# Performance work log

Measured on AMD Instinct MI355X. Metric: run time of the kernel, lower is better.

The kernel has to match this reference:

```python
import jax, jax.numpy as jnp
import numpy as np

B, T, O, H, CTX, HOR = 32, 24, 128, 512, 256, 48
MAX_STEP = 2.0


def setup_inputs() -> dict:
    key = jax.random.key(0)
    ks = jax.random.split(key, 20)
    def lin(k, out_d, in_d):
        bound = 1.0 / np.sqrt(in_d)
        kw, kb = jax.random.split(k)
        W = jax.random.uniform(kw, (out_d, in_d), jnp.float32, -bound, bound)
        b = jax.random.uniform(kb, (out_d,), jnp.float32, -bound, bound)
        return W, b
    W_emb, b_emb = lin(ks[0], H, 2)
    W_ctx, b_ctx = lin(ks[1], H, CTX)
    Wi_enc, bi_enc = lin(ks[2], 3 * H, H)
    Wh_enc, bh_enc = lin(ks[3], 3 * H, H)
    Wi_cell, bi_cell = lin(ks[4], 3 * H, H)
    Wh_cell, bh_cell = lin(ks[5], 3 * H, H)
    W1, b1 = lin(ks[6], H, H)
    W2, b2 = lin(ks[7], 2, H)
    z_ctx = jax.random.normal(ks[8], (B, CTX), jnp.float32)
    traj_hist = jax.random.uniform(ks[9], (B, T, O, 2), jnp.float32) * 10.0
    return dict(z_ctx=z_ctx, traj_hist=traj_hist,
                W_emb=W_emb, b_emb=b_emb, W_ctx=W_ctx, b_ctx=b_ctx,
                Wi_enc=Wi_enc, Wh_enc=Wh_enc, bi_enc=bi_enc, bh_enc=bh_enc,
                Wi_cell=Wi_cell, Wh_cell=Wh_cell, bi_cell=bi_cell, bh_cell=bh_cell,
                W1=W1, b1=b1, W2=W2, b2=b2, horizon=HOR)


def _gru(h, x, Wi, Wh, bi, bh):
    # PyTorch GRU gate math: gates ordered (r, z, n)
    gi = x @ Wi.T + bi  # [N, 3H]
    gh = h @ Wh.T + bh
    ir, iz, inn = jnp.split(gi, 3, axis=-1)
    hr, hz, hn = jnp.split(gh, 3, axis=-1)
    r = jax.nn.sigmoid(ir + hr)
    z = jax.nn.sigmoid(iz + hz)
    n = jnp.tanh(inn + r * hn)
    return (1.0 - z) * n + z * h


def reference(z_ctx, traj_hist, W_emb, b_emb, W_ctx, b_ctx,
              Wi_enc, Wh_enc, bi_enc, bh_enc,
              Wi_cell, Wh_cell, bi_cell, bh_cell,
              W1, b1, W2, b2, horizon):
    b, t, o, _ = traj_hist.shape
    Hd = W_emb.shape[0]
    seq = traj_hist.transpose(0, 2, 1, 3).reshape(b * o, t, 2)  # [N, t, 2]
    emb = seq @ W_emb.T + b_emb  # [N, t, H]

    h0 = jnp.zeros((b * o, Hd), traj_hist.dtype)
    def enc_step(h, x):
        return _gru(h, x, Wi_enc, Wh_enc, bi_enc, bh_enc), None
    h, _ = jax.lax.scan(enc_step, h0, emb.transpose(1, 0, 2))

    ctx = z_ctx @ W_ctx.T + b_ctx                         # [b, H]
    ctx = jnp.repeat(ctx[:, None, :], o, axis=1).reshape(b * o, Hd)
    h = h + ctx

    state0 = seq[:, -1]  # [N, 2]
    def dec_step(carry, _):
        h, state = carry
        inp = state @ W_emb.T + b_emb
        h = _gru(h, inp, Wi_cell, Wh_cell, bi_cell, bh_cell)
        d = jax.nn.gelu(h @ W1.T + b1, approximate=False) @ W2.T + b2  # [N, 2]
        d = MAX_STEP * jnp.tanh(d / MAX_STEP)
        s = state + d
        state = jnp.stack([jnp.clip(s[..., 0], -90.0, 90.0),
                           jnp.mod(s[..., 1], 360.0)], axis=-1)
        return (h, state), state
    _, outs = jax.lax.scan(dec_step, (h, state0), None, length=horizon)
    # outs: [horizon, N, 2] -> [b, horizon, o, 2]
    return outs.transpose(1, 0, 2).reshape(b, o, horizon, 2).transpose(0, 2, 1, 3)
```

## Files before the change

### kernel.cpp

```cpp
#include <hip/hip_runtime.h>
#include <hip/hip_bf16.h>
#include <math.h>

#define BB 32
#define TT 24
#define OO 128
#define HH 512
#define CTXD 256
#define HOR 48
#define NN (BB*OO)
#define G3 (3*HH)
#define KS 17

typedef unsigned short ushortt;
typedef __attribute__((ext_vector_type(8))) short bf16x8;
typedef __attribute__((ext_vector_type(4))) float f32x4;

__device__ __forceinline__ ushortt f2bf(float x) {
    union { float f; unsigned u; } v; v.f = x;
    unsigned r = v.u + 0x7FFF + ((v.u >> 16) & 1);
    return (ushortt)(r >> 16);
}
__device__ __forceinline__ float bf2f(ushortt b) {
    union { unsigned u; float f; } v; v.u = ((unsigned)b) << 16;
    return v.f;
}
__device__ __forceinline__ void splitbf(float x, ushortt& hi, ushortt& lo) {
    hi = f2bf(x);
    lo = f2bf(x - bf2f(hi));
}
__device__ __forceinline__ float sigm(float x) { return 1.f / (1.f + __expf(-x)); }
__device__ __forceinline__ float tanh_fast(float x) {
    float xc = fminf(fmaxf(x, -10.f), 10.f);
    float e = __expf(2.f * xc);
    return (e - 1.f) / (e + 1.f);
}



#define STEP_LOADA(Adst, ksv) do { \
  const size_t koff = (size_t)(ksv) * 512; \
  _Pragma("unroll") for (int mt_ = 0; mt_ < 2; mt_++) { \
    Adst[mt_*2+0] = *reinterpret_cast<const bf16x8*>(RAh + ao[mt_] + koff); \
    Adst[mt_*2+1] = *reinterpret_cast<const bf16x8*>(RAl + ao[mt_] + koff); \
  } } while(0)
#define STEP_LOADB(Bdst, ksv) do { \
  const size_t koff = (size_t)(ksv) * 512; \
  _Pragma("unroll") for (int i_ = 0; i_ < 6; i_++) { \
    Bdst[i_*2+0] = *reinterpret_cast<const bf16x8*>(Bh + bo[i_] + koff); \
    Bdst[i_*2+1] = *reinterpret_cast<const bf16x8*>(Bl + bo[i_] + koff); \
  } } while(0)
#define STEP_MFMA(Av, Bv) do { \
  _Pragma("unroll") for (int mt_ = 0; mt_ < 2; mt_++) \
  _Pragma("unroll") for (int i_ = 0; i_ < 6; i_++) \
    acc[mt_][i_] = __builtin_amdgcn_mfma_f32_16x16x32_bf16(Av[mt_*2+0], Bv[i_*2+0], acc[mt_][i_], 0,0,0); \
  _Pragma("unroll") for (int mt_ = 0; mt_ < 2; mt_++) \
  _Pragma("unroll") for (int i_ = 0; i_ < 6; i_++) \
    acc[mt_][i_] = __builtin_amdgcn_mfma_f32_16x16x32_bf16(Av[mt_*2+0], Bv[i_*2+1], acc[mt_][i_], 0,0,0); \
  _Pragma("unroll") for (int mt_ = 0; mt_ < 2; mt_++) \
  _Pragma("unroll") for (int i_ = 0; i_ < 6; i_++) \
    acc[mt_][i_] = __builtin_amdgcn_mfma_f32_16x16x32_bf16(Av[mt_*2+1], Bv[i_*2+0], acc[mt_][i_], 0,0,0); \
  } while(0)

template<bool ENC>
__global__ __launch_bounds__(256, 2) void step_kernel(
    const ushortt* __restrict__ RAh, const ushortt* __restrict__ RAl,
    ushortt* __restrict__ WAh, ushortt* __restrict__ WAl,
    const ushortt* __restrict__ Bh, const ushortt* __restrict__ Bl,
    const float* __restrict__ U, const float* __restrict__ cin,
    const float* __restrict__ xsrc, int t, const float* __restrict__ ctx)
{
    __shared__ float hbuf[128 * 36];
    const int mb = blockIdx.x >> 4;
    const int jb = blockIdx.x & 15;
    const int w = threadIdx.x >> 6, lane = threadIdx.x & 63;
    const int quad = lane >> 4, l15 = lane & 15;
    const int mtg = mb * 8 + w * 2;

    f32x4 acc[2][6];
#pragma unroll
    for (int a = 0; a < 2; a++)
#pragma unroll
        for (int b = 0; b < 6; b++) acc[a][b] = (f32x4){0.f,0.f,0.f,0.f};

    size_t ao[2];
    unsigned bo[6];
#pragma unroll
    for (int mt = 0; mt < 2; mt++) ao[mt] = (size_t)(mtg + mt) * (KS*512) + lane * 8;
#pragma unroll
    for (int g = 0; g < 3; g++)
#pragma unroll
        for (int jt = 0; jt < 2; jt++)
            bo[g*2+jt] = (unsigned)(g*32 + jb*2 + jt) * (KS*512) + lane * 8;

    bf16x8 aC[4], bC[12], aN[4], bN[12];
    STEP_LOADA(aC, 0); STEP_LOADB(bC, 0);
#pragma unroll 1
    for (int ks = 0; ks < 16; ks += 2) {
        STEP_LOADA(aN, ks+1); STEP_LOADB(bN, ks+1);
        STEP_MFMA(aC, bC);
        STEP_LOADA(aC, ks+2); STEP_LOADB(bC, ks+2);
        STEP_MFMA(aN, bN);
    }
    STEP_MFMA(aC, bC);

    const int jlo = jb * 32;
    float u0[2], u1[2], cc[2];
#pragma unroll
    for (int jt = 0; jt < 2; jt++) {
        int j = jlo + jt*16 + l15;
        u0[jt] = U[(1024 + j) * 2];
        u1[jt] = U[(1024 + j) * 2 + 1];
        cc[jt] = cin[1024 + j];
    }
    float x0v[2][4], x1v[2][4];
#pragma unroll
    for (int mt = 0; mt < 2; mt++)
#pragma unroll
        for (int reg = 0; reg < 4; reg++) {
            int row = (mtg + mt) * 16 + quad * 4 + reg;
            const float* p;
            if (ENC) p = xsrc + (((size_t)(row >> 7) * TT + t) * OO + (row & 127)) * 2;
            else     p = xsrc + (size_t)row * 2;
            x0v[mt][reg] = p[0]; x1v[mt][reg] = p[1];
        }
#pragma unroll
    for (int mt = 0; mt < 2; mt++)
#pragma unroll
        for (int jt = 0; jt < 2; jt++) {
            int qk = jt*2 + (l15 >> 3), slot = l15 & 7;
#pragma unroll
            for (int reg = 0; reg < 4; reg++) {
                int row = (mtg + mt) * 16 + quad * 4 + reg;
                float pr = acc[mt][0*2+jt][reg];
                float pz = acc[mt][1*2+jt][reg];
                float hn = acc[mt][2*2+jt][reg];
                size_t pos = (((size_t)(mtg + mt) * KS + jb) * 64 + qk*16 + quad*4 + reg) * 8 + slot;
                float hold = bf2f(RAh[pos]) + bf2f(RAl[pos]);
                float inn = fmaf(x1v[mt][reg], u1[jt], fmaf(x0v[mt][reg], u0[jt], cc[jt]));
                float rg = sigm(pr), zg = sigm(pz);
                float nn = tanh_fast(inn + rg * hn);
                float h = (1.f - zg) * nn + zg * hold;
                if (ENC && t == TT - 1) h += ctx[(size_t)(row >> 7) * HH + jlo + jt*16 + l15];
                hbuf[(w*32 + mt*16 + quad*4 + reg) * 36 + jt*16 + l15] = h;
            }
        }
    __syncthreads();
#pragma unroll
    for (int rr = 0; rr < 2; rr++) {
        int fr = threadIdx.x + 256 * rr;
        int mt8 = fr >> 6, fl = fr & 63;
        int qk = fl >> 4, rloc = mt8 * 16 + (fl & 15);
        const float* src = &hbuf[rloc * 36 + qk * 8];
        bf16x8 hv, lv;
#pragma unroll
        for (int s = 0; s < 8; s++) {
            ushortt hi, lo; splitbf(src[s], hi, lo);
            hv[s] = (short)hi; lv[s] = (short)lo;
        }
        size_t base = (((size_t)(mb*8 + mt8) * KS + jb) * 64 + fl) * 8;
        *reinterpret_cast<bf16x8*>(WAh + base) = hv;
        *reinterpret_cast<bf16x8*>(WAl + base) = lv;
    }
    if (ENC && jb == 0 && threadIdx.x < 128) {
        int row = mb * 128 + threadIdx.x;
        int tn = (t < TT - 1) ? (t + 1) : (TT - 1);
        const float* p = xsrc + (((size_t)(row >> 7) * TT + tn) * OO + (row & 127)) * 2;
        ushortt h0, l0, h1, l1;
        splitbf(p[0], h0, l0); splitbf(p[1], h1, l1);
        size_t xb = (((size_t)(row >> 4) * KS + 16) * 64 + (row & 15)) * 8;
        WAh[xb + 0] = h0; WAl[xb + 0] = l0;
        WAh[xb + 1] = h1; WAl[xb + 1] = l1;
    }
}

#define HEAD_LOADA(Adst, ksv) do { \
  const size_t koff = (size_t)(ksv) * 512; \
  _Pragma("unroll") for (int mt_ = 0; mt_ < 2; mt_++) { \
    Adst[mt_*2+0] = *reinterpret_cast<const bf16x8*>(Ah + hao[mt_] + koff); \
    Adst[mt_*2+1] = *reinterpret_cast<const bf16x8*>(Al + hao[mt_] + koff); \
  } } while(0)
#define HEAD_LOADB(Bdst, ksv) do { \
  const size_t koff = (size_t)(ksv) * 512; \
  _Pragma("unroll") for (int nt_ = 0; nt_ < 2; nt_++) { \
    Bdst[nt_*2+0] = *reinterpret_cast<const bf16x8*>(Bh + hbo[nt_] + koff); \
    Bdst[nt_*2+1] = *reinterpret_cast<const bf16x8*>(Bl + hbo[nt_] + koff); \
  } } while(0)
#define HEAD_MFMA(Av, Bv) do { \
  _Pragma("unroll") for (int mt_ = 0; mt_ < 2; mt_++) \
  _Pragma("unroll") for (int nt_ = 0; nt_ < 2; nt_++) { \
    acc[mt_][nt_] = __builtin_amdgcn_mfma_f32_16x16x32_bf16(Av[mt_*2+0], Bv[nt_*2+0], acc[mt_][nt_], 0,0,0); \
    acc[mt_][nt_] = __builtin_amdgcn_mfma_f32_16x16x32_bf16(Av[mt_*2+0], Bv[nt_*2+1], acc[mt_][nt_], 0,0,0); \
    acc[mt_][nt_] = __builtin_amdgcn_mfma_f32_16x16x32_bf16(Av[mt_*2+1], Bv[nt_*2+0], acc[mt_][nt_], 0,0,0); \
  } } while(0)

__global__ __launch_bounds__(256) void head_kernel(
    ushortt* Ah, ushortt* Al,
    const ushortt* __restrict__ Bh, const ushortt* __restrict__ Bl,
    const float* __restrict__ W2, const float* __restrict__ b2,
    float* __restrict__ d, unsigned* __restrict__ ctr,
    float* state, float* __restrict__ out, int t)
{
    const int mb = blockIdx.x >> 3;
    const int nb = blockIdx.x & 7;
    const int w = threadIdx.x >> 6, lane = threadIdx.x & 63;
    const int quad = lane >> 4, l15 = lane & 15;
    const int mtb = mb * 4 + (w & 1) * 2;
    const int ntb = nb * 4 + (w >> 1) * 2;

    f32x4 acc[2][2];
#pragma unroll
    for (int a = 0; a < 2; a++)
#pragma unroll
        for (int b = 0; b < 2; b++) acc[a][b] = (f32x4){0.f,0.f,0.f,0.f};

    size_t hao[2]; unsigned hbo[2];
#pragma unroll
    for (int mt = 0; mt < 2; mt++) hao[mt] = (size_t)(mtb + mt) * (KS*512) + lane * 8;
#pragma unroll
    for (int nt = 0; nt < 2; nt++) hbo[nt] = (unsigned)(ntb + nt) * (KS*512) + lane * 8;

    bf16x8 aC[4], bC[4], aN[4], bN[4];
    HEAD_LOADA(aC, 0); HEAD_LOADB(bC, 0);
#pragma unroll 1
    for (int ks = 0; ks < 16; ks += 2) {
        HEAD_LOADA(aN, ks+1); HEAD_LOADB(bN, ks+1);
        HEAD_MFMA(aC, bC);
        HEAD_LOADA(aC, ks+2); HEAD_LOADB(bC, ks+2);
        HEAD_MFMA(aN, bN);
    }
    HEAD_MFMA(aC, bC);

    float w2a[2], w2b[2];
#pragma unroll
    for (int nt = 0; nt < 2; nt++) {
        int col = (ntb + nt) * 16 + l15;
        w2a[nt] = W2[col]; w2b[nt] = W2[HH + col];
    }
    float p0[2][4], p1[2][4];
#pragma unroll
    for (int mt = 0; mt < 2; mt++)
#pragma unroll
        for (int reg = 0; reg < 4; reg++) { p0[mt][reg] = 0.f; p1[mt][reg] = 0.f; }
#pragma unroll
    for (int mt = 0; mt < 2; mt++)
#pragma unroll
        for (int nt = 0; nt < 2; nt++)
#pragma unroll
            for (int reg = 0; reg < 4; reg++) {
                float v = acc[mt][nt][reg];
                v = 0.5f * v * (1.0f + erff(v * 0.70710678118654752440f));
                p0[mt][reg] = fmaf(v, w2a[nt], p0[mt][reg]);
                p1[mt][reg] = fmaf(v, w2b[nt], p1[mt][reg]);
            }
#pragma unroll
    for (int m = 1; m < 16; m <<= 1)
#pragma unroll
        for (int mt = 0; mt < 2; mt++)
#pragma unroll
            for (int reg = 0; reg < 4; reg++) {
                p0[mt][reg] += __shfl_xor(p0[mt][reg], m, 64);
                p1[mt][reg] += __shfl_xor(p1[mt][reg], m, 64);
            }
    if (l15 == 0) {
#pragma unroll
        for (int mt = 0; mt < 2; mt++)
#pragma unroll
            for (int reg = 0; reg < 4; reg++) {
                int row = (mtb + mt) * 16 + quad * 4 + reg;
                atomicAdd(&d[row * 2], p0[mt][reg]);
                atomicAdd(&d[row * 2 + 1], p1[mt][reg]);
            }
    }

    __syncthreads();
    __shared__ unsigned lastv;
    if (threadIdx.x == 0) lastv = atomicAdd(ctr, 1u);
    __syncthreads();
    if (lastv == 511) {
        __threadfence();
#pragma unroll 1
        for (int rr = 0; rr < 16; rr++) {
            int row = rr * 256 + threadIdx.x;
            float d0 = d[row * 2]     + b2[0];
            float d1 = d[row * 2 + 1] + b2[1];
            d0 = 2.0f * tanhf(d0 * 0.5f);
            d1 = 2.0f * tanhf(d1 * 0.5f);
            float s0 = state[row * 2] + d0;
            s0 = fminf(fmaxf(s0, -90.f), 90.f);
            float s1 = state[row * 2 + 1] + d1;
            float rrm = fmodf(s1, 360.f);
            if (rrm < 0.f) rrm += 360.f;
            state[row * 2] = s0; state[row * 2 + 1] = rrm;
            float* op = out + (((size_t)(row >> 7) * HOR + t) * OO + (row & 127)) * 2;
            op[0] = s0; op[1] = rrm;
            ushortt h0, l0, h1, l1;
            splitbf(s0, h0, l0); splitbf(rrm, h1, l1);
            size_t xb = (((size_t)(row >> 4) * KS + 16) * 64 + (row & 15)) * 8;
            Ah[xb + 0] = h0; Al[xb + 0] = l0;
            Ah[xb + 1] = h1; Al[xb + 1] = l1;
        }
    }
}

__global__ void fuse_kernel(const float* __restrict__ Wi_enc, const float* __restrict__ bi_enc,
                            const float* __restrict__ Wi_cell, const float* __restrict__ bi_cell,
                            const float* __restrict__ W_emb, const float* __restrict__ b_emb,
                            float* __restrict__ Ue, float* __restrict__ ce,
                            float* __restrict__ Ud, float* __restrict__ cd) {
    int idx = blockIdx.x * 256 + threadIdx.x;
    if (idx >= 2 * G3) return;
    int which = idx / G3, j = idx % G3;
    const float* Wi = which ? Wi_cell : Wi_enc;
    const float* bi = which ? bi_cell : bi_enc;
    float u0 = 0.f, u1 = 0.f, cc = bi[j];
    for (int k = 0; k < HH; k++) {
        float w = Wi[(size_t)j * HH + k];
        u0 = fmaf(w, W_emb[k * 2 + 0], u0);
        u1 = fmaf(w, W_emb[k * 2 + 1], u1);
        cc = fmaf(w, b_emb[k], cc);
    }
    float* Uo = which ? Ud : Ue;
    float* cv = which ? cd : ce;
    Uo[j * 2 + 0] = u0; Uo[j * 2 + 1] = u1; cv[j] = cc;
}

__global__ void pack_frag(const float* __restrict__ W, const float* __restrict__ bhv,
                          const float* __restrict__ U, const float* __restrict__ cin,
                          const float* __restrict__ b1,
                          ushortt* __restrict__ Fh, ushortt* __restrict__ Fl, int N) {
    int idx = blockIdx.x * 256 + threadIdx.x;
    if (idx >= N * KS) return;
    int n = idx / KS, ks = idx % KS;
    int nt = n >> 4, l15 = n & 15;
    for (int kl = 0; kl < 32; kl++) {
        int k = ks * 32 + kl;
        float v = 0.f;
        if (k < 512) v = W[(size_t)n * 512 + k];
        else if (k == 512) v = (U && n < 1024) ? U[n * 2 + 0] : 0.f;
        else if (k == 513) v = (U && n < 1024) ? U[n * 2 + 1] : 0.f;
        else if (k == 514) v = U ? ((n < 1024) ? (cin[n] + bhv[n]) : bhv[n]) : b1[n];
        ushortt hi, lo; splitbf(v, hi, lo);
        int quad = kl >> 3, jj = kl & 7;
        size_t pos = ((size_t)(nt * KS + ks) * 64 + quad * 16 + l15) * 8 + jj;
        Fh[pos] = hi; Fl[pos] = lo;
    }
}

__global__ void ctx_kernel(const float* __restrict__ z, const float* __restrict__ Wc,
                           const float* __restrict__ bc, float* __restrict__ ctx) {
    int idx = blockIdx.x * 256 + threadIdx.x;
    int b = idx >> 9, j = idx & 511;
    float acc = bc[j];
    const float4* zp = (const float4*)(z + (size_t)b * CTXD);
    const float4* wp = (const float4*)(Wc + (size_t)j * CTXD);
    for (int k = 0; k < CTXD / 4; k++) {
        float4 a = zp[k], ww = wp[k];
        acc = fmaf(a.x, ww.x, fmaf(a.y, ww.y, fmaf(a.z, ww.z, fmaf(a.w, ww.w, acc))));
    }
    ctx[idx] = acc;
}

__global__ void init_kernel(const float* __restrict__ traj,
                            ushortt* __restrict__ Ah0, ushortt* __restrict__ Al0,
                            ushortt* __restrict__ Ah1, ushortt* __restrict__ Al1,
                            float* __restrict__ state, float* __restrict__ d,
                            unsigned* __restrict__ ctr) {
    int b = blockIdx.x;
    if (b < 1024) {
        int item = b * 256 + threadIdx.x;
        int mt = item >> 10, ks = (item >> 6) & 15, q4 = item & 63;
        size_t pos32 = ((size_t)(mt * KS + ks)) * 256 + q4 * 4;
        uint4 z = {0u,0u,0u,0u};
        *reinterpret_cast<uint4*>(((unsigned*)Ah0) + pos32) = z;
        *reinterpret_cast<uint4*>(((unsigned*)Al0) + pos32) = z;
    } else if (b < 1040) {
        int row = (b - 1024) * 256 + threadIdx.x;
        int bi = row >> 7, o = row & 127;
        const float* tp = traj + (((size_t)bi * TT + 0) * OO + o) * 2;
        ushortt xh0, xl0, xh1, xl1;
        splitbf(tp[0], xh0, xl0); splitbf(tp[1], xh1, xl1);
        for (int qk = 0; qk < 4; qk++)
            for (int slot = 0; slot < 8; slot++) {
                size_t p = (((size_t)(row >> 4) * KS + 16) * 64 + qk * 16 + (row & 15)) * 8 + slot;
                ushortt vh0 = 0, vl0 = 0, vh1 = 0;
                if (qk == 0 && slot == 0) { vh0 = xh0; vl0 = xl0; }
                else if (qk == 0 && slot == 1) { vh0 = xh1; vl0 = xl1; }
                else if (qk == 0 && slot == 2) { vh0 = 0x3F80; vh1 = 0x3F80; }
                Ah0[p] = vh0; Al0[p] = vl0; Ah1[p] = vh1; Al1[p] = 0;
            }
        const float* sp = traj + (((size_t)bi * TT + 23) * OO + o) * 2;
        state[row * 2] = sp[0]; state[row * 2 + 1] = sp[1];
    } else if (b < 1424) {
        int i = (b - 1040) * 256 + threadIdx.x;
        float4 z = {0.f,0.f,0.f,0.f};
        reinterpret_cast<float4*>(d)[i] = z;
    } else {
        if (threadIdx.x < 48) ctr[threadIdx.x] = 0u;
    }
}

extern "C" void kernel_launch(void* const* d_in, const int* in_sizes, int n_in,
                              void* d_out, int out_size, void* d_ws, size_t ws_size,
                              hipStream_t stream) {
    const float* z_ctx   = (const float*)d_in[0];
    const float* traj    = (const float*)d_in[1];
    const float* W_emb   = (const float*)d_in[2];
    const float* b_emb   = (const float*)d_in[3];
    const float* W_ctx   = (const float*)d_in[4];
    const float* b_ctx   = (const float*)d_in[5];
    const float* Wi_enc  = (const float*)d_in[6];
    const float* Wh_enc  = (const float*)d_in[7];
    const float* bi_enc  = (const float*)d_in[8];
    const float* bh_enc  = (const float*)d_in[9];
    const float* Wi_cell = (const float*)d_in[10];
    const float* Wh_cell = (const float*)d_in[11];
    const float* bi_cell = (const float*)d_in[12];
    const float* bh_cell = (const float*)d_in[13];
    const float* W1      = (const float*)d_in[14];
    const float* b1      = (const float*)d_in[15];
    const float* W2      = (const float*)d_in[16];
    const float* b2      = (const float*)d_in[17];
    float* out = (float*)d_out;

    char* ws = (char*)d_ws;
    size_t off = 0;
    auto alloc = [&](size_t bytes) { void* p = ws + off; off += (bytes + 255) & ~(size_t)255; return p; };
    const size_t hfrag = (size_t)256 * KS * 512 * 2;
    const size_t wfrag = (size_t)96  * KS * 512 * 2;
    const size_t w1frag = (size_t)32 * KS * 512 * 2;
    ushortt* Ah0 = (ushortt*)alloc(hfrag);
    ushortt* Al0 = (ushortt*)alloc(hfrag);
    ushortt* Ah1 = (ushortt*)alloc(hfrag);
    ushortt* Al1 = (ushortt*)alloc(hfrag);
    ushortt* WheH = (ushortt*)alloc(wfrag);
    ushortt* WheL = (ushortt*)alloc(wfrag);
    ushortt* WhdH = (ushortt*)alloc(wfrag);
    ushortt* WhdL = (ushortt*)alloc(wfrag);
    ushortt* W1H  = (ushortt*)alloc(w1frag);
    ushortt* W1L  = (ushortt*)alloc(w1frag);
    float*   state = (float*)alloc((size_t)NN * 2 * 4);
    float*   ctxb  = (float*)alloc((size_t)BB * HH * 4);
    float*   Ue    = (float*)alloc((size_t)G3 * 2 * 4);
    float*   ce    = (float*)alloc((size_t)G3 * 4);
    float*   Ud    = (float*)alloc((size_t)G3 * 2 * 4);
    float*   cd    = (float*)alloc((size_t)G3 * 4);
    float*   dbuf  = (float*)alloc((size_t)HOR * NN * 2 * 4);
    unsigned* ctr  = (unsigned*)alloc(HOR * 4);

    ushortt* bufAh[2] = {Ah0, Ah1};
    ushortt* bufAl[2] = {Al0, Al1};

    fuse_kernel<<<(2 * G3 + 255) / 256, 256, 0, stream>>>(Wi_enc, bi_enc, Wi_cell, bi_cell,
                                                          W_emb, b_emb, Ue, ce, Ud, cd);
    ctx_kernel<<<(BB * HH) / 256, 256, 0, stream>>>(z_ctx, W_ctx, b_ctx, ctxb);
    pack_frag<<<(G3 * KS + 255) / 256, 256, 0, stream>>>(Wh_enc, bh_enc, Ue, ce, nullptr, WheH, WheL, G3);
    pack_frag<<<(G3 * KS + 255) / 256, 256, 0, stream>>>(Wh_cell, bh_cell, Ud, cd, nullptr, WhdH, WhdL, G3);
    pack_frag<<<(HH * KS + 255) / 256, 256, 0, stream>>>(W1, nullptr, nullptr, nullptr, b1, W1H, W1L, HH);
    init_kernel<<<1425, 256, 0, stream>>>(traj, Ah0, Al0, Ah1, Al1, state, dbuf, ctr);

    for (int t = 0; t < TT; t++) {
        int rp = t & 1, wp = (t + 1) & 1;
        step_kernel<true><<<512, 256, 0, stream>>>(bufAh[rp], bufAl[rp], bufAh[wp], bufAl[wp],
                                                   WheH, WheL, Ue, ce, traj, t, ctxb);
    }
    for (int t = 0; t < HOR; t++) {
        int s = TT + t;
        int rp = s & 1, wp = (s + 1) & 1;
        step_kernel<false><<<512, 256, 0, stream>>>(bufAh[rp], bufAl[rp], bufAh[wp], bufAl[wp],
                                                    WhdH, WhdL, Ud, cd, state, t, nullptr);
        head_kernel<<<512, 256, 0, stream>>>(bufAh[wp], bufAl[wp], W1H, W1L, W2, b2,
                                             dbuf + (size_t)t * NN * 2, ctr + t, state, out, t);
    }
}
```

Measured before the change: 3.797 ms.

## Double per-block row tile in GRU step and head kernels, vectorize packing

Each step and head block now covers 256 rows instead of 128, with every wave computing four 16-row M tiles, so B-fragment loads are reused across more rows. Grids shrink to 256 blocks, occupancy drops to one block per SIMD group, and the head's last-block counter threshold changes to match. Weight packing now writes 8 contiguous elements per thread, and the LDS readback uses float4 loads. The trade is more registers per thread and fewer resident blocks, which weakens latency hiding on 256 CUs.

```diff
diff --git a/kernel.cpp b/kernel.cpp
--- a/kernel.cpp
+++ b/kernel.cpp
@@ -38,62 +38,60 @@
 
 
 
-#define STEP_LOADA(Adst, ksv) do { \
-  const size_t koff = (size_t)(ksv) * 512; \
-  _Pragma("unroll") for (int mt_ = 0; mt_ < 2; mt_++) { \
-    Adst[mt_*2+0] = *reinterpret_cast<const bf16x8*>(RAh + ao[mt_] + koff); \
-    Adst[mt_*2+1] = *reinterpret_cast<const bf16x8*>(RAl + ao[mt_] + koff); \
+#define STEP_LOADA(Ad, ksv) do { const size_t ko = (size_t)(ksv) * 512; \
+  _Pragma("unroll") for (int m_ = 0; m_ < 4; m_++) { \
+    Ad[m_*2+0] = *reinterpret_cast<const bf16x8*>(RAh + ao[m_] + ko); \
+    Ad[m_*2+1] = *reinterpret_cast<const bf16x8*>(RAl + ao[m_] + ko); \
   } } while(0)
-#define STEP_LOADB(Bdst, ksv) do { \
-  const size_t koff = (size_t)(ksv) * 512; \
+#define STEP_LOADB(Bd, ksv) do { const size_t ko = (size_t)(ksv) * 512; \
   _Pragma("unroll") for (int i_ = 0; i_ < 6; i_++) { \
-    Bdst[i_*2+0] = *reinterpret_cast<const bf16x8*>(Bh + bo[i_] + koff); \
-    Bdst[i_*2+1] = *reinterpret_cast<const bf16x8*>(Bl + bo[i_] + koff); \
+    Bd[i_*2+0] = *reinterpret_cast<const bf16x8*>(Bh + bo[i_] + ko); \
+    Bd[i_*2+1] = *reinterpret_cast<const bf16x8*>(Bl + bo[i_] + ko); \
   } } while(0)
 #define STEP_MFMA(Av, Bv) do { \
-  _Pragma("unroll") for (int mt_ = 0; mt_ < 2; mt_++) \
+  _Pragma("unroll") for (int m_ = 0; m_ < 4; m_++) \
   _Pragma("unroll") for (int i_ = 0; i_ < 6; i_++) \
-    acc[mt_][i_] = __builtin_amdgcn_mfma_f32_16x16x32_bf16(Av[mt_*2+0], Bv[i_*2+0], acc[mt_][i_], 0,0,0); \
-  _Pragma("unroll") for (int mt_ = 0; mt_ < 2; mt_++) \
+    acc[m_][i_] = __builtin_amdgcn_mfma_f32_16x16x32_bf16(Av[m_*2+0], Bv[i_*2+0], acc[m_][i_], 0,0,0); \
+  _Pragma("unroll") for (int m_ = 0; m_ < 4; m_++) \
   _Pragma("unroll") for (int i_ = 0; i_ < 6; i_++) \
-    acc[mt_][i_] = __builtin_amdgcn_mfma_f32_16x16x32_bf16(Av[mt_*2+0], Bv[i_*2+1], acc[mt_][i_], 0,0,0); \
-  _Pragma("unroll") for (int mt_ = 0; mt_ < 2; mt_++) \
+    acc[m_][i_] = __builtin_amdgcn_mfma_f32_16x16x32_bf16(Av[m_*2+0], Bv[i_*2+1], acc[m_][i_], 0,0,0); \
+  _Pragma("unroll") for (int m_ = 0; m_ < 4; m_++) \
   _Pragma("unroll") for (int i_ = 0; i_ < 6; i_++) \
-    acc[mt_][i_] = __builtin_amdgcn_mfma_f32_16x16x32_bf16(Av[mt_*2+1], Bv[i_*2+0], acc[mt_][i_], 0,0,0); \
+    acc[m_][i_] = __builtin_amdgcn_mfma_f32_16x16x32_bf16(Av[m_*2+1], Bv[i_*2+0], acc[m_][i_], 0,0,0); \
   } while(0)
 
 template<bool ENC>
-__global__ __launch_bounds__(256, 2) void step_kernel(
+__global__ __launch_bounds__(256, 1) void step_kernel(
     const ushortt* __restrict__ RAh, const ushortt* __restrict__ RAl,
     ushortt* __restrict__ WAh, ushortt* __restrict__ WAl,
     const ushortt* __restrict__ Bh, const ushortt* __restrict__ Bl,
     const float* __restrict__ U, const float* __restrict__ cin,
     const float* __restrict__ xsrc, int t, const float* __restrict__ ctx)
 {
-    __shared__ float hbuf[128 * 36];
+    __shared__ float hbuf[256 * 36];
     const int mb = blockIdx.x >> 4;
     const int jb = blockIdx.x & 15;
     const int w = threadIdx.x >> 6, lane = threadIdx.x & 63;
     const int quad = lane >> 4, l15 = lane & 15;
-    const int mtg = mb * 8 + w * 2;
-
-    f32x4 acc[2][6];
-#pragma unroll
-    for (int a = 0; a < 2; a++)
+    const int mtg = mb * 16 + w * 4;
+
+    f32x4 acc[4][6];
+#pragma unroll
+    for (int a = 0; a < 4; a++)
 #pragma unroll
         for (int b = 0; b < 6; b++) acc[a][b] = (f32x4){0.f,0.f,0.f,0.f};
 
-    size_t ao[2];
+    size_t ao[4];
     unsigned bo[6];
 #pragma unroll
-    for (int mt = 0; mt < 2; mt++) ao[mt] = (size_t)(mtg + mt) * (KS*512) + lane * 8;
+    for (int mt = 0; mt < 4; mt++) ao[mt] = (size_t)(mtg + mt) * (KS*512) + lane * 8;
 #pragma unroll
     for (int g = 0; g < 3; g++)
 #pragma unroll
         for (int jt = 0; jt < 2; jt++)
             bo[g*2+jt] = (unsigned)(g*32 + jb*2 + jt) * (KS*512) + lane * 8;
 
-    bf16x8 aC[4], bC[12], aN[4], bN[12];
+    bf16x8 aC[8], bC[12], aN[8], bN[12];
     STEP_LOADA(aC, 0); STEP_LOADB(bC, 0);
 #pragma unroll 1
     for (int ks = 0; ks < 16; ks += 2) {
@@ -113,9 +111,9 @@
         u1[jt] = U[(1024 + j) * 2 + 1];
         cc[jt] = cin[1024 + j];
     }
-    float x0v[2][4], x1v[2][4];
-#pragma unroll
-    for (int mt = 0; mt < 2; mt++)
+    float x0v[4][4], x1v[4][4];
+#pragma unroll
+    for (int mt = 0; mt < 4; mt++)
 #pragma unroll
         for (int reg = 0; reg < 4; reg++) {
             int row = (mtg + mt) * 16 + quad * 4 + reg;
@@ -125,7 +123,7 @@
             x0v[mt][reg] = p[0]; x1v[mt][reg] = p[1];
         }
 #pragma unroll
-    for (int mt = 0; mt < 2; mt++)
+    for (int mt = 0; mt < 4; mt++)
 #pragma unroll
         for (int jt = 0; jt < 2; jt++) {
             int qk = jt*2 + (l15 >> 3), slot = l15 & 7;
@@ -142,28 +140,30 @@
                 float nn = tanh_fast(inn + rg * hn);
                 float h = (1.f - zg) * nn + zg * hold;
                 if (ENC && t == TT - 1) h += ctx[(size_t)(row >> 7) * HH + jlo + jt*16 + l15];
-                hbuf[(w*32 + mt*16 + quad*4 + reg) * 36 + jt*16 + l15] = h;
+                hbuf[(w*64 + mt*16 + quad*4 + reg) * 36 + jt*16 + l15] = h;
             }
         }
     __syncthreads();
 #pragma unroll
-    for (int rr = 0; rr < 2; rr++) {
+    for (int rr = 0; rr < 4; rr++) {
         int fr = threadIdx.x + 256 * rr;
-        int mt8 = fr >> 6, fl = fr & 63;
-        int qk = fl >> 4, rloc = mt8 * 16 + (fl & 15);
-        const float* src = &hbuf[rloc * 36 + qk * 8];
+        int mt16 = fr >> 6, fl = fr & 63;
+        int qk = fl >> 4, rloc = mt16 * 16 + (fl & 15);
+        const float4 v0 = *reinterpret_cast<const float4*>(&hbuf[rloc * 36 + qk * 8]);
+        const float4 v1 = *reinterpret_cast<const float4*>(&hbuf[rloc * 36 + qk * 8 + 4]);
+        float src[8] = {v0.x, v0.y, v0.z, v0.w, v1.x, v1.y, v1.z, v1.w};
         bf16x8 hv, lv;
 #pragma unroll
         for (int s = 0; s < 8; s++) {
             ushortt hi, lo; splitbf(src[s], hi, lo);
             hv[s] = (short)hi; lv[s] = (short)lo;
         }
-        size_t base = (((size_t)(mb*8 + mt8) * KS + jb) * 64 + fl) * 8;
+        size_t base = (((size_t)(mb*16 + mt16) * KS + jb) * 64 + fl) * 8;
         *reinterpret_cast<bf16x8*>(WAh + base) = hv;
         *reinterpret_cast<bf16x8*>(WAl + base) = lv;
     }
-    if (ENC && jb == 0 && threadIdx.x < 128) {
-        int row = mb * 128 + threadIdx.x;
+    if (ENC && jb == 0) {
+        int row = mb * 256 + threadIdx.x;
         int tn = (t < TT - 1) ? (t + 1) : (TT - 1);
         const float* p = xsrc + (((size_t)(row >> 7) * TT + tn) * OO + (row & 127)) * 2;
         ushortt h0, l0, h1, l1;
@@ -174,53 +174,50 @@
     }
 }
 
-#define HEAD_LOADA(Adst, ksv) do { \
-  const size_t koff = (size_t)(ksv) * 512; \
-  _Pragma("unroll") for (int mt_ = 0; mt_ < 2; mt_++) { \
-    Adst[mt_*2+0] = *reinterpret_cast<const bf16x8*>(Ah + hao[mt_] + koff); \
-    Adst[mt_*2+1] = *reinterpret_cast<const bf16x8*>(Al + hao[mt_] + koff); \
+#define HEAD_LOADA(Ad, ksv) do { const size_t ko = (size_t)(ksv) * 512; \
+  _Pragma("unroll") for (int m_ = 0; m_ < 4; m_++) { \
+    Ad[m_*2+0] = *reinterpret_cast<const bf16x8*>(Ah + hao[m_] + ko); \
+    Ad[m_*2+1] = *reinterpret_cast<const bf16x8*>(Al + hao[m_] + ko); \
   } } while(0)
-#define HEAD_LOADB(Bdst, ksv) do { \
-  const size_t koff = (size_t)(ksv) * 512; \
-  _Pragma("unroll") for (int nt_ = 0; nt_ < 2; nt_++) { \
-    Bdst[nt_*2+0] = *reinterpret_cast<const bf16x8*>(Bh + hbo[nt_] + koff); \
-    Bdst[nt_*2+1] = *reinterpret_cast<const bf16x8*>(Bl + hbo[nt_] + koff); \
+#define HEAD_LOADB(Bd, ksv) do { const size_t ko = (size_t)(ksv) * 512; \
+  _Pragma("unroll") for (int n_ = 0; n_ < 2; n_++) { \
+    Bd[n_*2+0] = *reinterpret_cast<const bf16x8*>(Bh + hbo[n_] + ko); \
+    Bd[n_*2+1] = *reinterpret_cast<const bf16x8*>(Bl + hbo[n_] + ko); \
   } } while(0)
 #define HEAD_MFMA(Av, Bv) do { \
-  _Pragma("unroll") for (int mt_ = 0; mt_ < 2; mt_++) \
-  _Pragma("unroll") for (int nt_ = 0; nt_ < 2; nt_++) { \
-    acc[mt_][nt_] = __builtin_amdgcn_mfma_f32_16x16x32_bf16(Av[mt_*2+0], Bv[nt_*2+0], acc[mt_][nt_], 0,0,0); \
-    acc[mt_][nt_] = __builtin_amdgcn_mfma_f32_16x16x32_bf16(Av[mt_*2+0], Bv[nt_*2+1], acc[mt_][nt_], 0,0,0); \
-    acc[mt_][nt_] = __builtin_amdgcn_mfma_f32_16x16x32_bf16(Av[mt_*2+1], Bv[nt_*2+0], acc[mt_][nt_], 0,0,0); \
+  _Pragma("unroll") for (int m_ = 0; m_ < 4; m_++) \
+  _Pragma("unroll") for (int n_ = 0; n_ < 2; n_++) { \
+    acc[m_][n_] = __builtin_amdgcn_mfma_f32_16x16x32_bf16(Av[m_*2+0], Bv[n_*2+0], acc[m_][n_], 0,0,0); \
+    acc[m_][n_] = __builtin_amdgcn_mfma_f32_16x16x32_bf16(Av[m_*2+0], Bv[n_*2+1], acc[m_][n_], 0,0,0); \
+    acc[m_][n_] = __builtin_amdgcn_mfma_f32_16x16x32_bf16(Av[m_*2+1], Bv[n_*2+0], acc[m_][n_], 0,0,0); \
   } } while(0)
 
-__global__ __launch_bounds__(256) void head_kernel(
+__global__ __launch_bounds__(256, 1) void head_kernel(
     ushortt* Ah, ushortt* Al,
     const ushortt* __restrict__ Bh, const ushortt* __restrict__ Bl,
     const float* __restrict__ W2, const float* __restrict__ b2,
     float* __restrict__ d, unsigned* __restrict__ ctr,
     float* state, float* __restrict__ out, int t)
 {
-    const int mb = blockIdx.x >> 3;
-    const int nb = blockIdx.x & 7;
+    const int mb = blockIdx.x >> 4;
+    const int nb = blockIdx.x & 15;
     const int w = threadIdx.x >> 6, lane = threadIdx.x & 63;
     const int quad = lane >> 4, l15 = lane & 15;
-    const int mtb = mb * 4 + (w & 1) * 2;
-    const int ntb = nb * 4 + (w >> 1) * 2;
-
-    f32x4 acc[2][2];
-#pragma unroll
-    for (int a = 0; a < 2; a++)
+    const int mtg = mb * 16 + w * 4;
+
+    f32x4 acc[4][2];
+#pragma unroll
+    for (int a = 0; a < 4; a++)
 #pragma unroll
         for (int b = 0; b < 2; b++) acc[a][b] = (f32x4){0.f,0.f,0.f,0.f};
 
-    size_t hao[2]; unsigned hbo[2];
-#pragma unroll
-    for (int mt = 0; mt < 2; mt++) hao[mt] = (size_t)(mtb + mt) * (KS*512) + lane * 8;
-#pragma unroll
-    for (int nt = 0; nt < 2; nt++) hbo[nt] = (unsigned)(ntb + nt) * (KS*512) + lane * 8;
-
-    bf16x8 aC[4], bC[4], aN[4], bN[4];
+    size_t hao[4]; unsigned hbo[2];
+#pragma unroll
+    for (int mt = 0; mt < 4; mt++) hao[mt] = (size_t)(mtg + mt) * (KS*512) + lane * 8;
+#pragma unroll
+    for (int nt = 0; nt < 2; nt++) hbo[nt] = (unsigned)(nb*2 + nt) * (KS*512) + lane * 8;
+
+    bf16x8 aC[8], bC[4], aN[8], bN[4];
     HEAD_LOADA(aC, 0); HEAD_LOADB(bC, 0);
 #pragma unroll 1
     for (int ks = 0; ks < 16; ks += 2) {
@@ -234,16 +231,16 @@
     float w2a[2], w2b[2];
 #pragma unroll
     for (int nt = 0; nt < 2; nt++) {
-        int col = (ntb + nt) * 16 + l15;
+        int col = (nb*2 + nt) * 16 + l15;
         w2a[nt] = W2[col]; w2b[nt] = W2[HH + col];
     }
-    float p0[2][4], p1[2][4];
-#pragma unroll
-    for (int mt = 0; mt < 2; mt++)
+    float p0[4][4], p1[4][4];
+#pragma unroll
+    for (int mt = 0; mt < 4; mt++)
 #pragma unroll
         for (int reg = 0; reg < 4; reg++) { p0[mt][reg] = 0.f; p1[mt][reg] = 0.f; }
 #pragma unroll
-    for (int mt = 0; mt < 2; mt++)
+    for (int mt = 0; mt < 4; mt++)
 #pragma unroll
         for (int nt = 0; nt < 2; nt++)
 #pragma unroll
@@ -256,7 +253,7 @@
 #pragma unroll
     for (int m = 1; m < 16; m <<= 1)
 #pragma unroll
-        for (int mt = 0; mt < 2; mt++)
+        for (int mt = 0; mt < 4; mt++)
 #pragma unroll
             for (int reg = 0; reg < 4; reg++) {
                 p0[mt][reg] += __shfl_xor(p0[mt][reg], m, 64);
@@ -264,10 +261,10 @@
             }
     if (l15 == 0) {
 #pragma unroll
-        for (int mt = 0; mt < 2; mt++)
+        for (int mt = 0; mt < 4; mt++)
 #pragma unroll
             for (int reg = 0; reg < 4; reg++) {
-                int row = (mtb + mt) * 16 + quad * 4 + reg;
+                int row = (mtg + mt) * 16 + quad * 4 + reg;
                 atomicAdd(&d[row * 2], p0[mt][reg]);
                 atomicAdd(&d[row * 2 + 1], p1[mt][reg]);
             }
@@ -277,7 +274,7 @@
     __shared__ unsigned lastv;
     if (threadIdx.x == 0) lastv = atomicAdd(ctr, 1u);
     __syncthreads();
-    if (lastv == 511) {
+    if (lastv == 255) {
         __threadfence();
 #pragma unroll 1
         for (int rr = 0; rr < 16; rr++) {
@@ -330,21 +327,27 @@
                           const float* __restrict__ b1,
                           ushortt* __restrict__ Fh, ushortt* __restrict__ Fl, int N) {
     int idx = blockIdx.x * 256 + threadIdx.x;
-    if (idx >= N * KS) return;
-    int n = idx / KS, ks = idx % KS;
+    if (idx >= N * KS * 4) return;
+    int n = idx >> 6;
+    n = idx / (KS * 4);
+    int rem = idx - n * (KS * 4);
+    int ks = rem >> 2, quad = rem & 3;
     int nt = n >> 4, l15 = n & 15;
-    for (int kl = 0; kl < 32; kl++) {
-        int k = ks * 32 + kl;
+    ushortt hv[8], lv[8];
+#pragma unroll
+    for (int s = 0; s < 8; s++) {
+        int k = ks * 32 + quad * 8 + s;
         float v = 0.f;
         if (k < 512) v = W[(size_t)n * 512 + k];
         else if (k == 512) v = (U && n < 1024) ? U[n * 2 + 0] : 0.f;
         else if (k == 513) v = (U && n < 1024) ? U[n * 2 + 1] : 0.f;
         else if (k == 514) v = U ? ((n < 1024) ? (cin[n] + bhv[n]) : bhv[n]) : b1[n];
         ushortt hi, lo; splitbf(v, hi, lo);
-        int quad = kl >> 3, jj = kl & 7;
-        size_t pos = ((size_t)(nt * KS + ks) * 64 + quad * 16 + l15) * 8 + jj;
-        Fh[pos] = hi; Fl[pos] = lo;
-    }
+        hv[s] = hi; lv[s] = lo;
+    }
+    size_t pos = ((size_t)(nt * KS + ks) * 64 + quad * 16 + l15) * 8;
+#pragma unroll
+    for (int s = 0; s < 8; s++) { Fh[pos + s] = hv[s]; Fl[pos + s] = lv[s]; }
 }
 
 __global__ void ctx_kernel(const float* __restrict__ z, const float* __restrict__ Wc,
@@ -454,22 +457,22 @@
     fuse_kernel<<<(2 * G3 + 255) / 256, 256, 0, stream>>>(Wi_enc, bi_enc, Wi_cell, bi_cell,
                                                           W_emb, b_emb, Ue, ce, Ud, cd);
     ctx_kernel<<<(BB * HH) / 256, 256, 0, stream>>>(z_ctx, W_ctx, b_ctx, ctxb);
-    pack_frag<<<(G3 * KS + 255) / 256, 256, 0, stream>>>(Wh_enc, bh_enc, Ue, ce, nullptr, WheH, WheL, G3);
-    pack_frag<<<(G3 * KS + 255) / 256, 256, 0, stream>>>(Wh_cell, bh_cell, Ud, cd, nullptr, WhdH, WhdL, G3);
-    pack_frag<<<(HH * KS + 255) / 256, 256, 0, stream>>>(W1, nullptr, nullptr, nullptr, b1, W1H, W1L, HH);
+    pack_frag<<<(G3 * KS * 4 + 255) / 256, 256, 0, stream>>>(Wh_enc, bh_enc, Ue, ce, nullptr, WheH, WheL, G3);
+    pack_frag<<<(G3 * KS * 4 + 255) / 256, 256, 0, stream>>>(Wh_cell, bh_cell, Ud, cd, nullptr, WhdH, WhdL, G3);
+    pack_frag<<<(HH * KS * 4 + 255) / 256, 256, 0, stream>>>(W1, nullptr, nullptr, nullptr, b1, W1H, W1L, HH);
     init_kernel<<<1425, 256, 0, stream>>>(traj, Ah0, Al0, Ah1, Al1, state, dbuf, ctr);
 
     for (int t = 0; t < TT; t++) {
         int rp = t & 1, wp = (t + 1) & 1;
-        step_kernel<true><<<512, 256, 0, stream>>>(bufAh[rp], bufAl[rp], bufAh[wp], bufAl[wp],
+        step_kernel<true><<<256, 256, 0, stream>>>(bufAh[rp], bufAl[rp], bufAh[wp], bufAl[wp],
                                                    WheH, WheL, Ue, ce, traj, t, ctxb);
     }
     for (int t = 0; t < HOR; t++) {
         int s = TT + t;
         int rp = s & 1, wp = (s + 1) & 1;
-        step_kernel<false><<<512, 256, 0, stream>>>(bufAh[rp], bufAl[rp], bufAh[wp], bufAl[wp],
+        step_kernel<false><<<256, 256, 0, stream>>>(bufAh[rp], bufAl[rp], bufAh[wp], bufAl[wp],
                                                     WhdH, WhdL, Ud, cd, state, t, nullptr);
-        head_kernel<<<512, 256, 0, stream>>>(bufAh[wp], bufAl[wp], W1H, W1L, W2, b2,
+        head_kernel<<<256, 256, 0, stream>>>(bufAh[wp], bufAl[wp], W1H, W1L, W2, b2,
                                              dbuf + (size_t)t * NN * 2, ctr + t, state, out, t);
     }
 }
```

Measured after the change: 4.470 ms. 17.7% more time.
